# Performance work log

Hardware: AMD Instinct MI355X
Metric: run time of the kernel (lower is better)

The kernel has to match this reference:

```python
import jax, jax.numpy as jnp
import numpy as np

N = 1_000_000
D = 256
NUM_SEGMENTS = 4096  # = batch.max() + 1


def setup_inputs() -> dict:
    key = jax.random.key(0)
    ks = jax.random.split(key, 8)
    x = jax.random.normal(ks[0], (N, D), dtype=jnp.float32)
    batch = jnp.sort(jax.random.randint(ks[1], (N,), 0, NUM_SEGMENTS, dtype=jnp.int32))
    s = 1.0 / np.sqrt(D)
    s2 = 1.0 / np.sqrt(2 * D)
    W_in = jax.random.uniform(ks[2], (D, D), jnp.float32, -s, s)
    b_in = jax.random.uniform(ks[3], (D,), jnp.float32, -s, s)
    W1 = jax.random.uniform(ks[4], (D, 2 * D), jnp.float32, -s, s)
    b1 = jax.random.uniform(ks[5], (2 * D,), jnp.float32, -s, s)
    W2 = jax.random.uniform(ks[6], (2 * D, D), jnp.float32, -s2, s2)
    b2 = jax.random.uniform(ks[7], (D,), jnp.float32, -s2, s2)
    return {"x": x, "batch": batch, "W_in": W_in, "b_in": b_in,
            "W1": W1, "b1": b1, "W2": W2, "b2": b2}


def reference(x, batch, W_in, b_in, W1, b1, W2, b2):
    # proj_in: Linear(d, d)
    h = x @ W_in + b_in                                   # [N, D]
    # scatter_add segment-sum over batch ids -> [num_graphs, D]
    pooled = jax.ops.segment_sum(h, batch, num_segments=NUM_SEGMENTS)
    # proj_out: Linear(d, 2d) -> ReLU -> Linear(2d, d)
    out = jax.nn.relu(pooled @ W1 + b1) @ W2 + b2         # [num_graphs, D]
    return out
```

## Files before the change

kernel.cpp:

```cpp
#include <hip/hip_runtime.h>

#define DDIM 256
#define HDIM 512

typedef float f32x4 __attribute__((ext_vector_type(4)));
typedef short bf16x8 __attribute__((ext_vector_type(8)));

__device__ inline unsigned short f2bf(float f) {
  unsigned int u = __float_as_uint(f);
  u += 0x7fff + ((u >> 16) & 1);
  return (unsigned short)(u >> 16);
}

__global__ __launch_bounds__(256) void precompute_kernel(
    const float* __restrict__ W_in, const float* __restrict__ b_in,
    const float* __restrict__ W1, const float* __restrict__ W2,
    const int* __restrict__ batch, unsigned short* __restrict__ WfT,
    unsigned short* __restrict__ W2T, float* __restrict__ bvec,
    int* __restrict__ offsets, int N, int G) {
  const int b = blockIdx.x;
  if (b < 2 * DDIM + 2) {
    __shared__ float vrow[DDIM];
    const bool is_b = (b >= 2 * DDIM);
    const int i = is_b ? 0 : (b >> 1);
    const int half = is_b ? (b - 2 * DDIM) : (b & 1);
    const float* src = is_b ? b_in : (W_in + (size_t)i * DDIM);
    vrow[threadIdx.x] = src[threadIdx.x];
    __syncthreads();

    const int j = half * 256 + threadIdx.x;
    float h = 0.f;
#pragma unroll 8
    for (int k = 0; k < DDIM; ++k) h += vrow[k] * W1[(size_t)k * HDIM + j];
    if (is_b) bvec[j] = h;
    else WfT[(size_t)j * DDIM + i] = f2bf(h);
  } else if (b < 2 * DDIM + 2 + DDIM) {
    const int n = b - (2 * DDIM + 2);
    for (int k = threadIdx.x; k < HDIM; k += 256)
      W2T[(size_t)n * HDIM + k] = f2bf(W2[(size_t)k * DDIM + n]);
  } else {
    const int t = (b - (2 * DDIM + 2 + DDIM)) * 256 + threadIdx.x;
    if (t > G) return;
    int lo = 0, hi = N;
    while (lo < hi) {
      const int mid = (lo + hi) >> 1;
      if (batch[mid] < t) lo = mid + 1;
      else hi = mid;
    }
    offsets[t] = lo;
  }
}

__global__ __launch_bounds__(256) void segsum_kernel(
    const float* __restrict__ x, const int* __restrict__ offsets,
    unsigned short* __restrict__ Sb, float* __restrict__ counts) {
  const int g = blockIdx.x;
  const int start = offsets[g], end = offsets[g + 1];
  __shared__ float red[3][DDIM];

  const int w  = threadIdx.x >> 6;
  const int c4 = (threadIdx.x & 63) << 2;
  const float* xp = x + c4;

  f32x4 a0 = {0.f, 0.f, 0.f, 0.f};
  f32x4 a1 = {0.f, 0.f, 0.f, 0.f};
  f32x4 a2 = {0.f, 0.f, 0.f, 0.f};
  f32x4 a3 = {0.f, 0.f, 0.f, 0.f};

  int i = start + w;
  for (; i + 12 < end; i += 16) {
    const f32x4 v0 = __builtin_nontemporal_load(
        reinterpret_cast<const f32x4*>(xp + (size_t)i * DDIM));
    const f32x4 v1 = __builtin_nontemporal_load(
        reinterpret_cast<const f32x4*>(xp + (size_t)(i + 4) * DDIM));
    const f32x4 v2 = __builtin_nontemporal_load(
        reinterpret_cast<const f32x4*>(xp + (size_t)(i + 8) * DDIM));
    const f32x4 v3 = __builtin_nontemporal_load(
        reinterpret_cast<const f32x4*>(xp + (size_t)(i + 12) * DDIM));
    a0 += v0;
    a1 += v1;
    a2 += v2;
    a3 += v3;
  }
  for (; i < end; i += 4) {
    const f32x4 v0 = __builtin_nontemporal_load(
        reinterpret_cast<const f32x4*>(xp + (size_t)i * DDIM));
    a0 += v0;
  }
  a0 += a1;
  a2 += a3;
  a0 += a2;

  if (w != 0) *reinterpret_cast<f32x4*>(&red[w - 1][c4]) = a0;
  __syncthreads();
  if (w == 0) {
#pragma unroll
    for (int r = 0; r < 3; ++r) {
      a0 += *reinterpret_cast<const f32x4*>(&red[r][c4]);
    }
    ushort4 sv;
    sv.x = f2bf(a0.x);
    sv.y = f2bf(a0.y);
    sv.z = f2bf(a0.z);
    sv.w = f2bf(a0.w);
    *reinterpret_cast<ushort4*>(Sb + (size_t)g * DDIM + c4) = sv;
    if (threadIdx.x == 0) counts[g] = (float)(end - start);
  }
}

template <int K, bool RELU, int BIAS_MODE, bool OUTBF>
__global__ __launch_bounds__(256) void mfma_gemm_kernel(
    int N, const unsigned short* __restrict__ A,
    const unsigned short* __restrict__ BT, const float* __restrict__ bias,
    const float* __restrict__ bvec, const float* __restrict__ counts,
    float* __restrict__ Cf, unsigned short* __restrict__ Cb) {
  const int m0 = blockIdx.y * 64, n0 = blockIdx.x * 64;
  const int tid = threadIdx.x;
  const int wid = tid >> 6, lane = tid & 63;
  const int wr = wid >> 1, wc = wid & 1;
  const int l15 = lane & 15, lk8 = (lane >> 4) << 3;

  const unsigned short* Ap0 = A + (size_t)(m0 + wr * 32 + l15) * K + lk8;
  const unsigned short* Ap1 = Ap0 + (size_t)16 * K;
  const unsigned short* Bp0 = BT + (size_t)(n0 + wc * 32 + l15) * K + lk8;
  const unsigned short* Bp1 = Bp0 + (size_t)16 * K;

  f32x4 acc00 = {0.f, 0.f, 0.f, 0.f};
  f32x4 acc01 = {0.f, 0.f, 0.f, 0.f};
  f32x4 acc10 = {0.f, 0.f, 0.f, 0.f};
  f32x4 acc11 = {0.f, 0.f, 0.f, 0.f};

#pragma unroll
  for (int k0 = 0; k0 < K; k0 += 32) {
    const bf16x8 a0 = *reinterpret_cast<const bf16x8*>(Ap0 + k0);
    const bf16x8 a1 = *reinterpret_cast<const bf16x8*>(Ap1 + k0);
    const bf16x8 b0 = *reinterpret_cast<const bf16x8*>(Bp0 + k0);
    const bf16x8 b1 = *reinterpret_cast<const bf16x8*>(Bp1 + k0);
    acc00 = __builtin_amdgcn_mfma_f32_16x16x32_bf16(a0, b0, acc00, 0, 0, 0);
    acc01 = __builtin_amdgcn_mfma_f32_16x16x32_bf16(a0, b1, acc01, 0, 0, 0);
    acc10 = __builtin_amdgcn_mfma_f32_16x16x32_bf16(a1, b0, acc10, 0, 0, 0);
    acc11 = __builtin_amdgcn_mfma_f32_16x16x32_bf16(a1, b1, acc11, 0, 0, 0);
  }

  const int rbase = m0 + wr * 32 + ((lane >> 4) << 2);
  const int cbase = n0 + wc * 32 + l15;
#pragma unroll
  for (int si = 0; si < 2; ++si) {
#pragma unroll
    for (int sj = 0; sj < 2; ++sj) {
      const f32x4 ac = (si == 0) ? (sj == 0 ? acc00 : acc01)
                                 : (sj == 0 ? acc10 : acc11);
      const int col = cbase + sj * 16;
      const float bj = (BIAS_MODE >= 1) ? bias[col] : 0.f;
      const float vj = (BIAS_MODE == 2) ? bvec[col] : 0.f;
#pragma unroll
      for (int r = 0; r < 4; ++r) {
        const int row = rbase + si * 16 + r;
        float v = ac[r] + bj;
        if (BIAS_MODE == 2) v += counts[row] * vj;
        if (RELU) v = fmaxf(v, 0.f);
        if (OUTBF) Cb[(size_t)row * N + col] = f2bf(v);
        else       Cf[(size_t)row * N + col] = v;
      }
    }
  }
}

extern "C" void kernel_launch(void* const* d_in, const int* in_sizes, int n_in,
                              void* d_out, int out_size, void* d_ws,
                              size_t ws_size, hipStream_t stream) {
  const float* x     = (const float*)d_in[0];
  const int*   batch = (const int*)d_in[1];
  const float* W_in  = (const float*)d_in[2];
  const float* b_in  = (const float*)d_in[3];
  const float* W1    = (const float*)d_in[4];
  const float* b1    = (const float*)d_in[5];
  const float* W2    = (const float*)d_in[6];
  const float* b2    = (const float*)d_in[7];
  float* out = (float*)d_out;

  const int N = in_sizes[1];
  const int G = out_size / DDIM;

  char* wsb = (char*)d_ws;
  int* offsets = (int*)wsb;
  size_t off = (((size_t)(G + 1) * 4) + 63) & ~(size_t)63;
  unsigned short* WfT = (unsigned short*)(wsb + off);  off += (size_t)HDIM * DDIM * 2;
  unsigned short* W2T = (unsigned short*)(wsb + off);  off += (size_t)DDIM * HDIM * 2;
  float* bvec   = (float*)(wsb + off);                 off += (size_t)HDIM * 4;
  float* counts = (float*)(wsb + off);                 off += (size_t)G * 4;
  unsigned short* Sb = (unsigned short*)(wsb + off);   off += (size_t)G * DDIM * 2;
  unsigned short* Hb = (unsigned short*)(wsb + off);

  {
    const int nsearch = (G + 256) / 256;
    precompute_kernel<<<2 * DDIM + 2 + DDIM + nsearch, 256, 0, stream>>>(
        W_in, b_in, W1, W2, batch, WfT, W2T, bvec, offsets, N, G);
  }

  segsum_kernel<<<G, 256, 0, stream>>>(x, offsets, Sb, counts);

  mfma_gemm_kernel<DDIM, true, 2, true>
      <<<dim3(HDIM / 64, G / 64), 256, 0, stream>>>(
          HDIM, Sb, WfT, b1, bvec, counts, nullptr, Hb);

  mfma_gemm_kernel<HDIM, false, 1, false>
      <<<dim3(DDIM / 64, G / 64), 256, 0, stream>>>(
          DDIM, Hb, W2T, b2, nullptr, nullptr, out, nullptr);
}
```

Before: 194.4 us.

## Fuse weight precompute, segment offset search, and segment sum into one kernel

Merges the weight-folding/transposition kernel and the segment-sum kernel into a single launch. Each segment block now runs its own binary search over the sorted batch ids to find its start and end, instead of reading offsets written by a prior kernel. This removes one kernel launch and the offsets buffer, and lets the weight precompute overlap with the memory-bound segment reduction. In exchange, every segment block does two serial binary searches before it starts streaming rows, and the blocks from both stages now share one kernel's shared-memory footprint.

```diff
diff --git a/kernel.cpp b/kernel.cpp
--- a/kernel.cpp
+++ b/kernel.cpp
@@ -12,13 +12,15 @@
   return (unsigned short)(u >> 16);
 }
 
-__global__ __launch_bounds__(256) void precompute_kernel(
+__global__ __launch_bounds__(256) void fused_main_kernel(
+    const float* __restrict__ x, const int* __restrict__ batch,
     const float* __restrict__ W_in, const float* __restrict__ b_in,
     const float* __restrict__ W1, const float* __restrict__ W2,
-    const int* __restrict__ batch, unsigned short* __restrict__ WfT,
-    unsigned short* __restrict__ W2T, float* __restrict__ bvec,
-    int* __restrict__ offsets, int N, int G) {
+    unsigned short* __restrict__ WfT, unsigned short* __restrict__ W2T,
+    float* __restrict__ bvec, unsigned short* __restrict__ Sb,
+    float* __restrict__ counts, int N, int G) {
   const int b = blockIdx.x;
+
   if (b < 2 * DDIM + 2) {
     __shared__ float vrow[DDIM];
     const bool is_b = (b >= 2 * DDIM);
@@ -34,29 +36,31 @@
     for (int k = 0; k < DDIM; ++k) h += vrow[k] * W1[(size_t)k * HDIM + j];
     if (is_b) bvec[j] = h;
     else WfT[(size_t)j * DDIM + i] = f2bf(h);
-  } else if (b < 2 * DDIM + 2 + DDIM) {
+    return;
+  }
+  if (b < 2 * DDIM + 2 + DDIM) {
     const int n = b - (2 * DDIM + 2);
     for (int k = threadIdx.x; k < HDIM; k += 256)
       W2T[(size_t)n * HDIM + k] = f2bf(W2[(size_t)k * DDIM + n]);
-  } else {
-    const int t = (b - (2 * DDIM + 2 + DDIM)) * 256 + threadIdx.x;
-    if (t > G) return;
+    return;
+  }
+
+  const int g = b - (2 * DDIM + 2 + DDIM);
+  __shared__ int se[2];
+  __shared__ float red[3][DDIM];
+
+  if (threadIdx.x < 2) {
+    const int target = g + threadIdx.x;
     int lo = 0, hi = N;
     while (lo < hi) {
       const int mid = (lo + hi) >> 1;
-      if (batch[mid] < t) lo = mid + 1;
+      if (batch[mid] < target) lo = mid + 1;
       else hi = mid;
     }
-    offsets[t] = lo;
-  }
-}
-
-__global__ __launch_bounds__(256) void segsum_kernel(
-    const float* __restrict__ x, const int* __restrict__ offsets,
-    unsigned short* __restrict__ Sb, float* __restrict__ counts) {
-  const int g = blockIdx.x;
-  const int start = offsets[g], end = offsets[g + 1];
-  __shared__ float red[3][DDIM];
+    se[threadIdx.x] = lo;
+  }
+  __syncthreads();
+  const int start = se[0], end = se[1];
 
   const int w  = threadIdx.x >> 6;
   const int c4 = (threadIdx.x & 63) << 2;
@@ -183,8 +187,7 @@
   const int G = out_size / DDIM;
 
   char* wsb = (char*)d_ws;
-  int* offsets = (int*)wsb;
-  size_t off = (((size_t)(G + 1) * 4) + 63) & ~(size_t)63;
+  size_t off = 0;
   unsigned short* WfT = (unsigned short*)(wsb + off);  off += (size_t)HDIM * DDIM * 2;
   unsigned short* W2T = (unsigned short*)(wsb + off);  off += (size_t)DDIM * HDIM * 2;
   float* bvec   = (float*)(wsb + off);                 off += (size_t)HDIM * 4;
@@ -192,13 +195,8 @@
   unsigned short* Sb = (unsigned short*)(wsb + off);   off += (size_t)G * DDIM * 2;
   unsigned short* Hb = (unsigned short*)(wsb + off);
 
-  {
-    const int nsearch = (G + 256) / 256;
-    precompute_kernel<<<2 * DDIM + 2 + DDIM + nsearch, 256, 0, stream>>>(
-        W_in, b_in, W1, W2, batch, WfT, W2T, bvec, offsets, N, G);
-  }
-
-  segsum_kernel<<<G, 256, 0, stream>>>(x, offsets, Sb, counts);
+  fused_main_kernel<<<2 * DDIM + 2 + DDIM + G, 256, 0, stream>>>(
+      x, batch, W_in, b_in, W1, W2, WfT, W2T, bvec, Sb, counts, N, G);
 
   mfma_gemm_kernel<DDIM, true, 2, true>
       <<<dim3(HDIM / 64, G / 64), 256, 0, stream>>>(
```

Result: faster. 190.0 us (-2.3%).
